# Kernel optimization log

Measured on AMD Instinct MI355X. Metric: run time of the kernel, lower is better.

Reference implementation:

```python
import jax, jax.numpy as jnp
import numpy as np
from jax import lax

EPS = 1e-8  # numerical safety in squash sqrt (torch repo uses plain sqrt)

def squash(s, axis=-1):
    sq = jnp.sum(s * s, axis=axis, keepdims=True)
    return (sq / (1.0 + sq)) * s / jnp.sqrt(sq + EPS)

def conv2d(x, w, b, stride):
    y = lax.conv_general_dilated(x, w, (stride, stride), 'VALID',
                                 dimension_numbers=('NCHW', 'OIHW', 'NCHW'))
    return y + b[None, :, None, None]

def setup_inputs() -> dict:
    key = jax.random.key(0)
    ks = jax.random.split(key, 12)
    B = 256
    x = jax.random.normal(ks[0], (B, 1, 28, 28), dtype=jnp.float32)
    conv_w = jax.random.normal(ks[1], (256, 1, 9, 9), dtype=jnp.float32) * 0.05
    conv_b = jnp.zeros((256,), dtype=jnp.float32)
    caps1_w = jax.random.normal(ks[2], (32, 8, 256, 9, 9), dtype=jnp.float32) * 0.01
    caps1_b = jnp.zeros((32, 8), dtype=jnp.float32)
    caps2_w = jax.random.normal(ks[3], (10, 1152, 8, 16), dtype=jnp.float32)  # torch.randn
    dec_w1 = jax.random.normal(ks[4], (160, 512), dtype=jnp.float32) * 0.05
    dec_b1 = jnp.zeros((512,), dtype=jnp.float32)
    dec_w2 = jax.random.normal(ks[5], (512, 1024), dtype=jnp.float32) * 0.04
    dec_b2 = jnp.zeros((1024,), dtype=jnp.float32)
    dec_w3 = jax.random.normal(ks[6], (1024, 784), dtype=jnp.float32) * 0.03
    dec_b3 = jnp.zeros((784,), dtype=jnp.float32)
    return {"x": x, "conv_w": conv_w, "conv_b": conv_b, "caps1_w": caps1_w,
            "caps1_b": caps1_b, "caps2_w": caps2_w, "dec_w1": dec_w1,
            "dec_b1": dec_b1, "dec_w2": dec_w2, "dec_b2": dec_b2,
            "dec_w3": dec_w3, "dec_b3": dec_b3}

def reference(x, conv_w, conv_b, caps1_w, caps1_b, caps2_w,
              dec_w1, dec_b1, dec_w2, dec_b2, dec_w3, dec_b3):
    B = x.shape[0]
    # conv + relu -> [B,256,20,20]
    h = jax.nn.relu(conv2d(x, conv_w, conv_b, 1))
    # CapsLayerOne: 32 parallel convs folded into one grouped-out conv -> [B,256,6,6]
    u = conv2d(h, caps1_w.reshape(32 * 8, 256, 9, 9), caps1_b.reshape(-1), 2)
    u = u.reshape(B, 32, 8, 6, 6)                    # [B,caps,ch,h,w]
    # replicate torch cat(dim=-1).view(B,8,-1): flatten order (h, caps, w) per channel
    u = u.transpose(0, 2, 3, 1, 4).reshape(B, 8, 1152)  # [B,8,N]
    u = squash(u.transpose(0, 2, 1))                 # [B,N,8], N=1152
    # CapsLayerTwo dynamic routing
    x_hat = jnp.einsum('bni,cnio->cbno', u, caps2_w)[:, :, :, None, :]  # [10,B,N,1,16]
    b = jnp.zeros_like(x_hat)
    v = None
    for i in range(3):
        c = jax.nn.softmax(b, axis=2)
        s = jnp.sum(x_hat * c, axis=2, keepdims=True)  # [10,B,1,1,16]
        v = squash(s)
        if i != 2:
            b = b + jnp.sum(x_hat * v, axis=-1, keepdims=True)
    v = v[:, :, 0, 0, :].transpose(1, 0, 2)            # [B,10,16]
    class_scores = jnp.sqrt(jnp.sum(v * v, axis=-1) + EPS)  # [B,10]
    class_probabilities = jax.nn.softmax(class_scores, axis=-1)
    labels = jnp.argmax(class_probabilities, axis=1)
    y = jax.nn.one_hot(labels, 10, dtype=v.dtype)
    masked = (v * y[:, :, None]).reshape(B, 160)
    d = jax.nn.relu(masked @ dec_w1 + dec_b1)
    d = jax.nn.relu(d @ dec_w2 + dec_b2)
    reconstructions = jax.nn.sigmoid(d @ dec_w3 + dec_b3)  # [B,784]
    return (class_probabilities, reconstructions)
```

## Files before the change

kernel.cpp:

```cpp
#include <hip/hip_runtime.h>
#include <cstdint>
#include <cstddef>

#define EPSF 1e-8f

typedef __attribute__((ext_vector_type(8))) short bf16x8;
typedef __attribute__((ext_vector_type(4))) float f32x4;
typedef unsigned short ushort_t;

static __device__ __forceinline__ ushort_t f2bf(float f) {
  unsigned u = __builtin_bit_cast(unsigned, f);
  unsigned r = (u + 0x7FFFu + ((u >> 16) & 1u)) >> 16;
  return (ushort_t)r;
}
static __device__ __forceinline__ float bf2f(ushort_t h) {
  return __builtin_bit_cast(float, (unsigned)h << 16);
}

__global__ __launch_bounds__(256) void conv1_kernel(
    const float* __restrict__ x, const float* __restrict__ cw,
    const float* __restrict__ cb, ushort_t* __restrict__ h2x)
{
  int oy = blockIdx.x, b = blockIdx.y, ci = threadIdx.x;
  float w[81];
#pragma unroll
  for (int i = 0; i < 81; ++i) w[i] = cw[ci * 81 + i];
  float bias = cb[ci];
  float acc[20];
#pragma unroll
  for (int ox = 0; ox < 20; ++ox) acc[ox] = bias;
  const float* xb = x + (size_t)b * 784;
  for (int ky = 0; ky < 9; ++ky) {
    const float* row = xb + (oy + ky) * 28;
    float rv[28];
#pragma unroll
    for (int c = 0; c < 28; ++c) rv[c] = row[c];
#pragma unroll
    for (int kx = 0; kx < 9; ++kx) {
      float wv = w[ky * 9 + kx];
#pragma unroll
      for (int ox = 0; ox < 20; ++ox)
        acc[ox] = fmaf(rv[ox + kx], wv, acc[ox]);
    }
  }
  int cblk = ci >> 5, jj = ci & 31;
#pragma unroll
  for (int ox = 0; ox < 20; ++ox) {
    float a = fmaxf(acc[ox], 0.f);
    ushort_t hi = f2bf(a);
    ushort_t lo = f2bf(a - bf2f(hi));
    size_t o = ((size_t)(b * 400 + oy * 20 + ox)) * 512 + cblk * 64 + jj;
    h2x[o] = hi; h2x[o + 32] = lo;
  }
}

__global__ __launch_bounds__(256) void w2k_prep_kernel(
    const float* __restrict__ c1w, ushort_t* __restrict__ w2k)
{
  int co = blockIdx.x, ci = threadIdx.x;
  const float* src = c1w + ((size_t)co * 256 + ci) * 81;
  int cblk = ci >> 5, jj = ci & 31;
  for (int tap = 0; tap < 81; ++tap) {
    float v = src[tap];
    ushort_t hi = f2bf(v);
    size_t dst = ((size_t)co * 81 + tap) * 512 + cblk * 64 + jj;
    w2k[dst] = hi;
    w2k[dst + 32] = f2bf(v - bf2f(hi));
  }
}

__global__ __launch_bounds__(256, 2) void caps1_mfma_kernel(
    const ushort_t* __restrict__ h2x, const ushort_t* __restrict__ w2k,
    float* __restrict__ partial)
{
  int bid = blockIdx.x;
  int ks = bid & 3;
  int nt = (bid >> 2) & 1;
  int kt = (bid >> 3) & 1;
  int mt = (bid >> 4) & 1;
  int pos = bid >> 5;
  int ys = pos / 6, xs = pos % 6;
  int t = threadIdx.x;
  int wid = t >> 6, lane = t & 63;
  int wr = wid >> 1, wc = wid & 1;
  int lrow = lane & 15, g = lane >> 4;

  int b0 = mt * 128, n0 = nt * 128;
  int tb    = kt ? 41 : 0;
  int ntaps = kt ? 40 : 41;
  int nht   = 2 * ntaps;

  __shared__ ushort_t lds[2][2][128 * 64];

  f32x4 acc[4][4];
#pragma unroll
  for (int i = 0; i < 4; ++i)
#pragma unroll
    for (int j = 0; j < 4; ++j) acc[i][j] = (f32x4){0.f, 0.f, 0.f, 0.f};

  int c_ = (t & 7) ^ ((t >> 3) & 7);
  size_t aRow400[4], bRow81[4];
  int ldsBase[4];
#pragma unroll
  for (int i = 0; i < 4; ++i) {
    int row = i * 32 + (t >> 3);
    aRow400[i] = (size_t)(b0 + row) * 400;
    bRow81[i]  = (size_t)(n0 + row) * 81;
    ldsBase[i] = (i * 32 + wid * 8) * 64;
  }

  auto stage = [&](int j, int bufi) {
    int tap = tb + (j >> 1);
    int cbk = ks * 2 + (j & 1);
    int ky = tap / 9, kx = tap - ky * 9;
    int pix = (2 * ys + ky) * 20 + 2 * xs + kx;
    int sub = cbk * 64 + c_ * 8;
#pragma unroll
    for (int i = 0; i < 4; ++i) {
      const ushort_t* ga = h2x + (aRow400[i] + pix) * 512 + sub;
      const ushort_t* gb = w2k + (bRow81[i] + tap) * 512 + sub;
      __builtin_amdgcn_global_load_lds(ga, &lds[bufi][0][ldsBase[i]], 16, 0, 0);
      __builtin_amdgcn_global_load_lds(gb, &lds[bufi][1][ldsBase[i]], 16, 0, 0);
    }
  };

  bf16x8 a_h[4], a_l[4], b_h[4], b_l[4];
  auto read_frags = [&](int bufi) {
    const ushort_t* LA = &lds[bufi][0][0];
    const ushort_t* LB = &lds[bufi][1][0];
#pragma unroll
    for (int f = 0; f < 4; ++f) {
      int ra = wr * 64 + f * 16 + lrow;
      int sa = ra * 64;
      a_h[f] = *(const bf16x8*)(LA + sa + ((g)     ^ (ra & 7)) * 8);
      a_l[f] = *(const bf16x8*)(LA + sa + ((4 + g) ^ (ra & 7)) * 8);
      int rb = wc * 64 + f * 16 + lrow;
      int sb = rb * 64;
      b_h[f] = *(const bf16x8*)(LB + sb + ((g)     ^ (rb & 7)) * 8);
      b_l[f] = *(const bf16x8*)(LB + sb + ((4 + g) ^ (rb & 7)) * 8);
    }
  };

  stage(0, 0);
  stage(1, 1);
  asm volatile("s_waitcnt vmcnt(8)" ::: "memory");
  __builtin_amdgcn_sched_barrier(0);
  __builtin_amdgcn_s_barrier();

  for (int j = 0; j < nht; ++j) {
    int cur = j & 1;
    read_frags(cur);
    asm volatile("s_waitcnt lgkmcnt(0)" ::: "memory");
    __builtin_amdgcn_sched_barrier(0);
    __builtin_amdgcn_s_barrier();

    if (j + 2 < nht) stage(j + 2, cur);
    __builtin_amdgcn_sched_barrier(0);

    __builtin_amdgcn_s_setprio(1);
#pragma unroll
    for (int mf = 0; mf < 4; ++mf)
#pragma unroll
      for (int nf = 0; nf < 4; ++nf) {
        acc[mf][nf] = __builtin_amdgcn_mfma_f32_16x16x32_bf16(a_h[mf], b_h[nf], acc[mf][nf], 0, 0, 0);
        acc[mf][nf] = __builtin_amdgcn_mfma_f32_16x16x32_bf16(a_h[mf], b_l[nf], acc[mf][nf], 0, 0, 0);
        acc[mf][nf] = __builtin_amdgcn_mfma_f32_16x16x32_bf16(a_l[mf], b_h[nf], acc[mf][nf], 0, 0, 0);
      }
    __builtin_amdgcn_s_setprio(0);
    __builtin_amdgcn_sched_barrier(0);

    if (j + 2 < nht) { asm volatile("s_waitcnt vmcnt(8)" ::: "memory"); }
    else             { asm volatile("s_waitcnt vmcnt(0)" ::: "memory"); }
    __builtin_amdgcn_sched_barrier(0);
    __builtin_amdgcn_s_barrier();
  }

  float* pp = partial + (size_t)(kt * 4 + ks) * 2359296;
#pragma unroll
  for (int mf = 0; mf < 4; ++mf) {
    int m = b0 + wr * 64 + mf * 16 + g * 4;
#pragma unroll
    for (int nf = 0; nf < 4; ++nf) {
      int n = n0 + wc * 64 + nf * 16 + lrow;
#pragma unroll
      for (int r = 0; r < 4; ++r)
        pp[((size_t)(pos * 256 + m + r)) * 256 + n] = acc[mf][nf][r];
    }
  }
}

__global__ __launch_bounds__(256) void combine_kernel(
    const float* __restrict__ partial, const float* __restrict__ c1b, float* __restrict__ u)
{
  int gidx = blockIdx.x * 256 + threadIdx.x;
  int caps = gidx & 31;
  int b = (gidx >> 5) & 255;
  int pos = gidx >> 13;
  int ys = pos / 6, xs = pos % 6;
  size_t base = ((size_t)pos * 256 + b) * 256 + caps * 8;
  f32x4 s0 = {0.f, 0.f, 0.f, 0.f}, s1 = {0.f, 0.f, 0.f, 0.f};
#pragma unroll
  for (int ksp = 0; ksp < 8; ++ksp) {
    const float* pp = partial + (size_t)ksp * 2359296 + base;
    s0 += *(const f32x4*)pp;
    s1 += *(const f32x4*)(pp + 4);
  }
  const float* bp = c1b + caps * 8;
#pragma unroll
  for (int i = 0; i < 4; ++i) { s0[i] += bp[i]; s1[i] += bp[4 + i]; }
  float sq = s0[0]*s0[0] + s0[1]*s0[1] + s0[2]*s0[2] + s0[3]*s0[3]
           + s1[0]*s1[0] + s1[1]*s1[1] + s1[2]*s1[2] + s1[3]*s1[3];
  float scale = sq / ((1.f + sq) * sqrtf(sq + EPSF));
  int nvec = ys * 192 + caps * 6 + xs;
  float* up = u + ((size_t)b * 1152 + nvec) * 8;
  f32x4 o0, o1;
#pragma unroll
  for (int i = 0; i < 4; ++i) { o0[i] = s0[i] * scale; o1[i] = s1[i] * scale; }
  *(f32x4*)up = o0;
  *(f32x4*)(up + 4) = o1;
}

__global__ __launch_bounds__(320) void xhat_kernel(
    const float* __restrict__ u, const float* __restrict__ W2, float* __restrict__ xh)
{
  int np = blockIdx.x;
  int t = threadIdx.x;
  int c  = t >> 5;
  int nh = (t >> 4) & 1;
  int o  = t & 15;
  int n = np * 2 + nh;
  __shared__ float us[2][256][8];
  for (int e = t; e < 4096; e += 320) {
    int b = e >> 4;
    int nn = (e >> 3) & 1, i = e & 7;
    us[nn][b][i] = u[((size_t)b * 1152 + np * 2 + nn) * 8 + i];
  }
  __syncthreads();
  float wcol[8];
  const float* wp = W2 + (((size_t)c * 1152 + n) * 8) * 16 + o;
#pragma unroll
  for (int i = 0; i < 8; ++i) wcol[i] = wp[i * 16];
  float* xp = xh + ((size_t)(c * 256) * 1152 + n) * 16 + o;
  for (int b = 0; b < 256; ++b) {
    float s = 0.f;
#pragma unroll
    for (int i = 0; i < 8; ++i) s = fmaf(us[nh][b][i], wcol[i], s);
    xp[(size_t)b * 1152 * 16] = s;
  }
}

__global__ __launch_bounds__(256) void routing_kernel(
    const float* __restrict__ xhat, float* __restrict__ vout)
{
  int b = blockIdx.x, c = blockIdx.y, t = threadIdx.x;
  int wid = t >> 6, lane = t & 63;
  float xh[5][16];
  float bn[5] = {0, 0, 0, 0, 0};
  bool valid[5];
  const float* xp = xhat + ((size_t)(c * 256 + b)) * 1152 * 16;
#pragma unroll
  for (int j = 0; j < 5; ++j) {
    int n = t + 256 * j;
    valid[j] = (n < 1152);
    if (valid[j]) {
      const f32x4* q = (const f32x4*)(xp + (size_t)n * 16);
#pragma unroll
      for (int v4 = 0; v4 < 4; ++v4) {
        f32x4 val = q[v4];
#pragma unroll
        for (int k = 0; k < 4; ++k) xh[j][v4 * 4 + k] = val[k];
      }
    } else {
#pragma unroll
      for (int o = 0; o < 16; ++o) xh[j][o] = 0.f;
    }
  }
  __shared__ float redm[4], redz[4], reds[64], sv[16];
  float scale = 0.f;
  for (int it = 0; it < 3; ++it) {
    float m = -1e30f;
#pragma unroll
    for (int j = 0; j < 5; ++j) if (valid[j]) m = fmaxf(m, bn[j]);
    for (int d = 1; d < 64; d <<= 1) m = fmaxf(m, __shfl_xor(m, d));
    if (lane == 0) redm[wid] = m;
    __syncthreads();
    m = fmaxf(fmaxf(redm[0], redm[1]), fmaxf(redm[2], redm[3]));
    float e[5]; float z = 0.f;
#pragma unroll
    for (int j = 0; j < 5; ++j) { e[j] = valid[j] ? expf(bn[j] - m) : 0.f; z += e[j]; }
    for (int d = 1; d < 64; d <<= 1) z += __shfl_xor(z, d);
    if (lane == 0) redz[wid] = z;
    __syncthreads();
    z = redz[0] + redz[1] + redz[2] + redz[3];
    float ps[16];
#pragma unroll
    for (int o = 0; o < 16; ++o) ps[o] = 0.f;
#pragma unroll
    for (int j = 0; j < 5; ++j)
#pragma unroll
      for (int o = 0; o < 16; ++o) ps[o] = fmaf(e[j], xh[j][o], ps[o]);
#pragma unroll
    for (int o = 0; o < 16; ++o) {
      float vv = ps[o];
      for (int d = 1; d < 64; d <<= 1) vv += __shfl_xor(vv, d);
      if (lane == 0) reds[wid * 16 + o] = vv;
    }
    __syncthreads();
    if (t < 16) sv[t] = (reds[t] + reds[16 + t] + reds[32 + t] + reds[48 + t]) / z;
    __syncthreads();
    float vsc[16]; float sq = 0.f;
#pragma unroll
    for (int o = 0; o < 16; ++o) { vsc[o] = sv[o]; sq += sv[o] * sv[o]; }
    scale = sq / ((1.f + sq) * sqrtf(sq + EPSF));
    if (it < 2) {
#pragma unroll
      for (int j = 0; j < 5; ++j) if (valid[j]) {
        float dot = 0.f;
#pragma unroll
        for (int o = 0; o < 16; ++o) dot = fmaf(xh[j][o], vsc[o] * scale, dot);
        bn[j] += dot;
      }
    }
    __syncthreads();
  }
  if (t < 16) vout[((size_t)c * 256 + b) * 16 + t] = sv[t] * scale;
}

__global__ __launch_bounds__(256) void classify_kernel(
    const float* __restrict__ v, float* __restrict__ probs, float* __restrict__ masked)
{
  int b = blockIdx.x, t = threadIdx.x;
  __shared__ float sc[10], vv[160];
  int c = t >> 4, o = t & 15;
  float val = 0.f;
  if (t < 160) { val = v[((size_t)c * 256 + b) * 16 + o]; vv[t] = val; }
  float sq = val * val;
  sq += __shfl_xor(sq, 1); sq += __shfl_xor(sq, 2);
  sq += __shfl_xor(sq, 4); sq += __shfl_xor(sq, 8);
  if (t < 160 && o == 0) sc[c] = sqrtf(sq + EPSF);
  __syncthreads();
  float m = sc[0];
#pragma unroll
  for (int i = 1; i < 10; ++i) m = fmaxf(m, sc[i]);
  float ee[10]; float Z = 0.f;
#pragma unroll
  for (int i = 0; i < 10; ++i) { ee[i] = expf(sc[i] - m); Z += ee[i]; }
  float p[10];
#pragma unroll
  for (int i = 0; i < 10; ++i) p[i] = ee[i] / Z;
  int label = 0; float best = p[0];
#pragma unroll
  for (int i = 1; i < 10; ++i) if (p[i] > best) { best = p[i]; label = i; }
  if (t < 10) probs[(size_t)b * 10 + t] = p[t];
  if (t < 160) masked[(size_t)b * 160 + t] = (c == label) ? vv[t] : 0.f;
}

template <int ACT>
__global__ __launch_bounds__(256) void mlp_kernel(
    const float* __restrict__ A, const float* __restrict__ W,
    const float* __restrict__ bias, float* __restrict__ C, int N, int K)
{
  int j = blockIdx.x * 64 + (threadIdx.x & 63);
  int ty = threadIdx.x >> 6;
  int m0 = blockIdx.y * 16;
  __shared__ float As[16][33];
  float acc[4] = {0.f, 0.f, 0.f, 0.f};
  for (int k0 = 0; k0 < K; k0 += 32) {
    for (int e = threadIdx.x; e < 512; e += 256) {
      int r = e >> 5, kk = e & 31;
      As[r][kk] = A[(size_t)(m0 + r) * K + k0 + kk];
    }
    __syncthreads();
    if (j < N) {
      for (int kk = 0; kk < 32; ++kk) {
        float wv = W[(size_t)(k0 + kk) * N + j];
#pragma unroll
        for (int r = 0; r < 4; ++r) acc[r] = fmaf(As[ty + 4 * r][kk], wv, acc[r]);
      }
    }
    __syncthreads();
  }
  if (j < N) {
    float bv = bias[j];
#pragma unroll
    for (int r = 0; r < 4; ++r) {
      float xx = acc[r] + bv;
      if (ACT == 0) xx = fmaxf(xx, 0.f);
      else xx = 1.f / (1.f + expf(-xx));
      C[(size_t)(m0 + ty + 4 * r) * N + j] = xx;
    }
  }
}

extern "C" void kernel_launch(void* const* d_in, const int* in_sizes, int n_in,
                              void* d_out, int out_size, void* d_ws, size_t ws_size,
                              hipStream_t stream)
{
  const float* x   = (const float*)d_in[0];
  const float* cw  = (const float*)d_in[1];
  const float* cb  = (const float*)d_in[2];
  const float* c1w = (const float*)d_in[3];
  const float* c1b = (const float*)d_in[4];
  const float* c2w = (const float*)d_in[5];
  const float* w1  = (const float*)d_in[6];
  const float* b1  = (const float*)d_in[7];
  const float* w2  = (const float*)d_in[8];
  const float* b2  = (const float*)d_in[9];
  const float* w3  = (const float*)d_in[10];
  const float* b3  = (const float*)d_in[11];
  float* out = (float*)d_out;

  char* p = (char*)d_ws;
  float* xh = (float*)p;
  ushort_t* h2x = (ushort_t*)p; p += (size_t)52428800 * 2;
  ushort_t* w2k = (ushort_t*)p; p += (size_t)10616832 * 2;
  float* partial = (float*)p;   p += (size_t)8 * 2359296 * 4;
  float* u       = (float*)p;   p += (size_t)2359296 * 4;
  float* v       = (float*)p;   p += (size_t)40960 * 4;
  float* masked  = (float*)p;   p += (size_t)40960 * 4;
  float* a1      = (float*)p;   p += (size_t)131072 * 4;
  float* a2      = (float*)p;   p += (size_t)262144 * 4;

  hipLaunchKernelGGL(w2k_prep_kernel, dim3(256), dim3(256), 0, stream, c1w, w2k);
  hipLaunchKernelGGL(conv1_kernel, dim3(20, 256), dim3(256), 0, stream, x, cw, cb, h2x);
  hipLaunchKernelGGL(caps1_mfma_kernel, dim3(1152), dim3(256), 0, stream, h2x, w2k, partial);
  hipLaunchKernelGGL(combine_kernel, dim3(1152), dim3(256), 0, stream, partial, c1b, u);
  hipLaunchKernelGGL(xhat_kernel, dim3(576), dim3(320), 0, stream, u, c2w, xh);
  hipLaunchKernelGGL(routing_kernel, dim3(256, 10), dim3(256), 0, stream, xh, v);
  hipLaunchKernelGGL(classify_kernel, dim3(256), dim3(256), 0, stream, v, out, masked);
  hipLaunchKernelGGL(mlp_kernel<0>, dim3(8, 16), dim3(256), 0, stream, masked, w1, b1, a1, 512, 160);
  hipLaunchKernelGGL(mlp_kernel<0>, dim3(16, 16), dim3(256), 0, stream, a1, w2, b2, a2, 1024, 512);
  hipLaunchKernelGGL(mlp_kernel<1>, dim3(13, 16), dim3(256), 0, stream, a2, w3, b3, out + 2560, 784, 1024);
}
```

Before: 609.9 us.

## Load B weight fragments directly from global into registers, bypassing LDS

```diff
diff --git a/kernel.cpp b/kernel.cpp
--- a/kernel.cpp
+++ b/kernel.cpp
@@ -90,7 +90,7 @@
   int ntaps = kt ? 40 : 41;
   int nht   = 2 * ntaps;
 
-  __shared__ ushort_t lds[2][2][128 * 64];
+  __shared__ ushort_t lds[2][128 * 64];
 
   f32x4 acc[4][4];
 #pragma unroll
@@ -99,78 +99,103 @@
     for (int j = 0; j < 4; ++j) acc[i][j] = (f32x4){0.f, 0.f, 0.f, 0.f};
 
   int c_ = (t & 7) ^ ((t >> 3) & 7);
-  size_t aRow400[4], bRow81[4];
+  size_t aRow400[4];
   int ldsBase[4];
 #pragma unroll
   for (int i = 0; i < 4; ++i) {
     int row = i * 32 + (t >> 3);
     aRow400[i] = (size_t)(b0 + row) * 400;
-    bRow81[i]  = (size_t)(n0 + row) * 81;
     ldsBase[i] = (i * 32 + wid * 8) * 64;
   }
 
-  auto stage = [&](int j, int bufi) {
+  auto stageA = [&](int j, int bufi) {
     int tap = tb + (j >> 1);
-    int cbk = ks * 2 + (j & 1);
     int ky = tap / 9, kx = tap - ky * 9;
     int pix = (2 * ys + ky) * 20 + 2 * xs + kx;
-    int sub = cbk * 64 + c_ * 8;
-#pragma unroll
-    for (int i = 0; i < 4; ++i) {
-      const ushort_t* ga = h2x + (aRow400[i] + pix) * 512 + sub;
-      const ushort_t* gb = w2k + (bRow81[i] + tap) * 512 + sub;
-      __builtin_amdgcn_global_load_lds(ga, &lds[bufi][0][ldsBase[i]], 16, 0, 0);
-      __builtin_amdgcn_global_load_lds(gb, &lds[bufi][1][ldsBase[i]], 16, 0, 0);
-    }
+    int sub = ks * 128 + (j & 1) * 64 + c_ * 8;
+#pragma unroll
+    for (int i = 0; i < 4; ++i)
+      __builtin_amdgcn_global_load_lds(h2x + (aRow400[i] + pix) * 512 + sub,
+                                       &lds[bufi][ldsBase[i]], 16, 0, 0);
   };
 
-  bf16x8 a_h[4], a_l[4], b_h[4], b_l[4];
-  auto read_frags = [&](int bufi) {
-    const ushort_t* LA = &lds[bufi][0][0];
-    const ushort_t* LB = &lds[bufi][1][0];
+  const ushort_t* bBase[4];
+#pragma unroll
+  for (int nf = 0; nf < 4; ++nf)
+    bBase[nf] = w2k + (size_t)(n0 + wc * 64 + nf * 16 + lrow) * 81 * 512
+                + ks * 128 + g * 8;
+
+  auto loadB = [&](int j, bf16x8 (&bh)[4], bf16x8 (&bl)[4]) {
+    int tap = tb + (j >> 1);
+    size_t off = (size_t)tap * 512 + (size_t)(j & 1) * 64;
+#pragma unroll
+    for (int nf = 0; nf < 4; ++nf) {
+      bh[nf] = *(const bf16x8*)(bBase[nf] + off);
+      bl[nf] = *(const bf16x8*)(bBase[nf] + off + 32);
+    }
+  };
+
+  bf16x8 a_h[4], a_l[4];
+  auto readA = [&](int bufi) {
+    const ushort_t* LA = &lds[bufi][0];
 #pragma unroll
     for (int f = 0; f < 4; ++f) {
       int ra = wr * 64 + f * 16 + lrow;
       int sa = ra * 64;
       a_h[f] = *(const bf16x8*)(LA + sa + ((g)     ^ (ra & 7)) * 8);
       a_l[f] = *(const bf16x8*)(LA + sa + ((4 + g) ^ (ra & 7)) * 8);
-      int rb = wc * 64 + f * 16 + lrow;
-      int sb = rb * 64;
-      b_h[f] = *(const bf16x8*)(LB + sb + ((g)     ^ (rb & 7)) * 8);
-      b_l[f] = *(const bf16x8*)(LB + sb + ((4 + g) ^ (rb & 7)) * 8);
     }
   };
 
-  stage(0, 0);
-  stage(1, 1);
-  asm volatile("s_waitcnt vmcnt(8)" ::: "memory");
+  auto mfmaC = [&](bf16x8 (&bh)[4], bf16x8 (&bl)[4]) {
+    __builtin_amdgcn_s_setprio(1);
+#pragma unroll
+    for (int mf = 0; mf < 4; ++mf)
+#pragma unroll
+      for (int nf = 0; nf < 4; ++nf) {
+        acc[mf][nf] = __builtin_amdgcn_mfma_f32_16x16x32_bf16(a_h[mf], bh[nf], acc[mf][nf], 0, 0, 0);
+        acc[mf][nf] = __builtin_amdgcn_mfma_f32_16x16x32_bf16(a_h[mf], bl[nf], acc[mf][nf], 0, 0, 0);
+        acc[mf][nf] = __builtin_amdgcn_mfma_f32_16x16x32_bf16(a_l[mf], bh[nf], acc[mf][nf], 0, 0, 0);
+      }
+    __builtin_amdgcn_s_setprio(0);
+  };
+
+  bf16x8 B0h[4], B0l[4], B1h[4], B1l[4];
+
+  stageA(0, 0);
+  loadB(0, B0h, B0l);
+  stageA(1, 1);
+  loadB(1, B1h, B1l);
+  asm volatile("s_waitcnt vmcnt(12)" ::: "memory");
   __builtin_amdgcn_sched_barrier(0);
   __builtin_amdgcn_s_barrier();
 
-  for (int j = 0; j < nht; ++j) {
-    int cur = j & 1;
-    read_frags(cur);
+  for (int j = 0; j < nht; j += 2) {
+    bool pf = (j + 2 < nht);
+    readA(0);
     asm volatile("s_waitcnt lgkmcnt(0)" ::: "memory");
     __builtin_amdgcn_sched_barrier(0);
     __builtin_amdgcn_s_barrier();
-
-    if (j + 2 < nht) stage(j + 2, cur);
-    __builtin_amdgcn_sched_barrier(0);
-
-    __builtin_amdgcn_s_setprio(1);
-#pragma unroll
-    for (int mf = 0; mf < 4; ++mf)
-#pragma unroll
-      for (int nf = 0; nf < 4; ++nf) {
-        acc[mf][nf] = __builtin_amdgcn_mfma_f32_16x16x32_bf16(a_h[mf], b_h[nf], acc[mf][nf], 0, 0, 0);
-        acc[mf][nf] = __builtin_amdgcn_mfma_f32_16x16x32_bf16(a_h[mf], b_l[nf], acc[mf][nf], 0, 0, 0);
-        acc[mf][nf] = __builtin_amdgcn_mfma_f32_16x16x32_bf16(a_l[mf], b_h[nf], acc[mf][nf], 0, 0, 0);
-      }
-    __builtin_amdgcn_s_setprio(0);
-    __builtin_amdgcn_sched_barrier(0);
-
-    if (j + 2 < nht) { asm volatile("s_waitcnt vmcnt(8)" ::: "memory"); }
-    else             { asm volatile("s_waitcnt vmcnt(0)" ::: "memory"); }
+    if (pf) stageA(j + 2, 0);
+    __builtin_amdgcn_sched_barrier(0);
+    mfmaC(B0h, B0l);
+    if (pf) loadB(j + 2, B0h, B0l);
+    __builtin_amdgcn_sched_barrier(0);
+    if (pf) { asm volatile("s_waitcnt vmcnt(12)" ::: "memory"); }
+    else    { asm volatile("s_waitcnt vmcnt(0)"  ::: "memory"); }
+    __builtin_amdgcn_sched_barrier(0);
+    __builtin_amdgcn_s_barrier();
+    readA(1);
+    asm volatile("s_waitcnt lgkmcnt(0)" ::: "memory");
+    __builtin_amdgcn_sched_barrier(0);
+    __builtin_amdgcn_s_barrier();
+    if (pf) stageA(j + 3, 1);
+    __builtin_amdgcn_sched_barrier(0);
+    mfmaC(B1h, B1l);
+    if (pf) loadB(j + 3, B1h, B1l);
+    __builtin_amdgcn_sched_barrier(0);
+    if (pf) { asm volatile("s_waitcnt vmcnt(12)" ::: "memory"); }
+    else    { asm volatile("s_waitcnt vmcnt(0)"  ::: "memory"); }
     __builtin_amdgcn_sched_barrier(0);
     __builtin_amdgcn_s_barrier();
   }
```

New measurement: 799.6 us. 31.1% more time.
